# Optimization experiments

Hardware: AMD Instinct MI355X
Metric: run time of the kernel (lower is better)

The kernel has to match this reference:

```python
import jax, jax.numpy as jnp
import numpy as np
from jax import lax

B, L = 4, 1024
D_MODEL, D_STATE, D_CONV = 512, 16, 4
D_INNER = 2 * D_MODEL          # expand=2
DT_RANK = D_MODEL // 16        # ceil(512/16)=32
K_EXPERTS = 2                  # num_experts_per_token; only first k experts are used
EPS = 1e-5


def setup_inputs() -> dict:
    key = jax.random.key(0)
    ks = jax.random.split(key, 14)
    def n(k, shape, scale=0.02):
        return jax.random.normal(k, shape, jnp.float32) * scale
    # Mamba S4D-real init for A: A_log = log(1..d_state) broadcast over channels
    A_log = jnp.log(jnp.broadcast_to(jnp.arange(1, D_STATE + 1, dtype=jnp.float32), (D_INNER, D_STATE)))
    return {
        "x": jax.random.normal(ks[0], (B, L, D_MODEL), jnp.float32),
        "in_proj_w": n(ks[1], (2 * D_INNER, D_MODEL)),
        "conv_w": n(ks[2], (D_INNER, 1, D_CONV), 0.1),
        "conv_b": n(ks[3], (D_INNER,), 0.1),
        "x_proj_w": n(ks[4], (DT_RANK + 2 * D_STATE, D_INNER)),
        "dt_proj_w": n(ks[5], (D_INNER, DT_RANK), 0.1),
        "dt_proj_b": n(ks[6], (D_INNER,), 0.1),
        "A_log": A_log,
        "D_skip": jnp.ones((D_INNER,), jnp.float32),
        "out_proj_w": n(ks[7], (D_MODEL, D_INNER)),
        "moe_w1": n(ks[8], (K_EXPERTS, 2 * D_MODEL, D_MODEL)),
        "moe_b1": n(ks[9], (K_EXPERTS, 2 * D_MODEL)),
        "moe_w2": n(ks[10], (K_EXPERTS, D_MODEL, 2 * D_MODEL)),
        "moe_b2": n(ks[11], (K_EXPERTS, D_MODEL)),
    }


def _layernorm(x):
    # fresh nn.LayerNorm each forward: weight=1, bias=0, eps=1e-5
    mu = jnp.mean(x, -1, keepdims=True)
    var = jnp.mean(jnp.square(x - mu), -1, keepdims=True)
    return (x - mu) / jnp.sqrt(var + EPS)


def _mamba(x, in_proj_w, conv_w, conv_b, x_proj_w, dt_proj_w, dt_proj_b, A_log, D_skip, out_proj_w):
    b = x.shape[0]
    xz = x @ in_proj_w.T                               # (b, L, 2*d_inner)
    xc, z = jnp.split(xz, 2, axis=-1)
    # causal depthwise conv1d (torch pads both sides with d_conv-1 then slices [:L])
    conv = lax.conv_general_dilated(
        xc.transpose(0, 2, 1), conv_w, (1,), [(D_CONV - 1, 0)],
        feature_group_count=D_INNER) + conv_b[None, :, None]
    xs = jax.nn.silu(conv).transpose(0, 2, 1)          # (b, L, d_inner)
    dbc = xs @ x_proj_w.T                              # (b, L, dt_rank + 2*d_state)
    dt = dbc[..., :DT_RANK]
    Bm = dbc[..., DT_RANK:DT_RANK + D_STATE]           # (b, L, d_state)
    Cm = dbc[..., DT_RANK + D_STATE:]                  # (b, L, d_state)
    delta = jax.nn.softplus(dt @ dt_proj_w.T + dt_proj_b)  # (b, L, d_inner)
    A = -jnp.exp(A_log)                                # (d_inner, d_state)
    dA = jnp.exp(jnp.einsum('bld,dn->bldn', delta, A))     # (b, L, d_inner, d_state)
    dBx = (delta * xs)[..., None] * Bm[:, :, None, :]       # (b, L, d_inner, d_state)

    def step(h, inp):
        dA_t, dBx_t, C_t = inp
        h = dA_t * h + dBx_t                           # (b, d_inner, d_state)
        y = jnp.einsum('bdn,bn->bd', h, C_t)
        return h, y

    h0 = jnp.zeros((b, D_INNER, D_STATE), x.dtype)
    _, ys = lax.scan(step, h0, (dA.transpose(1, 0, 2, 3), dBx.transpose(1, 0, 2, 3), Cm.transpose(1, 0, 2)))
    y = ys.transpose(1, 0, 2) + xs * D_skip            # (b, L, d_inner)
    y = y * jax.nn.silu(z)
    return y @ out_proj_w.T                            # (b, L, d_model)


def reference(x, in_proj_w, conv_w, conv_b, x_proj_w, dt_proj_w, dt_proj_b,
              A_log, D_skip, out_proj_w, moe_w1, moe_b1, moe_w2, moe_b2):
    skip = x
    h = _layernorm(x)
    h = _mamba(h, in_proj_w, conv_w, conv_b, x_proj_w, dt_proj_w, dt_proj_b, A_log, D_skip, out_proj_w) + h
    h = _layernorm(h)
    # static 'MoE': unweighted average of the first K_EXPERTS dense FFNs
    a = jax.nn.relu(jnp.einsum('bld,ekd->belk', h, moe_w1) + moe_b1[None, :, None, :])
    moe = jnp.einsum('belk,edk->beld', a, moe_w2) + moe_b2[None, :, None, :]
    return jnp.mean(moe, axis=1) + skip
```

## Files before the change

kernel.cpp:

```cpp
#include <hip/hip_runtime.h>
#include <hip/hip_bf16.h>

#define BB 4
#define LL 1024
#define DM 512
#define DI 1024
#define DS 16
#define DTR 32
#define MM (BB*LL)

#define ACT_NONE 0
#define ACT_RELU 1
#define ACT_SP   2

#define CHUNK 128
#define NCH (LL/CHUNK)
#define NSTATE 65536

typedef __attribute__((ext_vector_type(8))) __bf16 bf16x8;
typedef __attribute__((ext_vector_type(8))) unsigned short us8;
typedef __attribute__((ext_vector_type(4))) float f32x4;

__device__ __forceinline__ unsigned short f2bf(float f) {
  union { float f; unsigned int u; } a; a.f = f;
  unsigned int r = a.u + 0x7fffu + ((a.u >> 16) & 1u);
  return (unsigned short)(r >> 16);
}

__device__ __forceinline__ bf16x8 ld_frag(const unsigned short* p) {
  us8 s = *(const us8*)p;
  return __builtin_bit_cast(bf16x8, s);
}

__device__ __forceinline__ void gload16(const void* g, void* l) {
  __builtin_amdgcn_global_load_lds(
      (const __attribute__((address_space(1))) void*)g,
      (__attribute__((address_space(3))) void*)l, 16, 0, 0);
}

__global__ __launch_bounds__(256) void f2b4_kernel(const float* __restrict__ in,
                                                   unsigned short* __restrict__ out, int n4) {
  int i = blockIdx.x * 256 + threadIdx.x;
  if (i < n4) {
    float4 v = ((const float4*)in)[i];
    ushort4 o;
    o.x = f2bf(v.x); o.y = f2bf(v.y); o.z = f2bf(v.z); o.w = f2bf(v.w);
    ((ushort4*)out)[i] = o;
  }
}

__global__ __launch_bounds__(256) void repack_kernel(
    const float* __restrict__ moe_w2, const float* __restrict__ moe_b2,
    unsigned short* __restrict__ w2catb, float* __restrict__ b2avg)
{
  int idx = blockIdx.x * 256 + threadIdx.x;
  if (idx < DM * 2*DI) {
    int nrow = idx >> 11;
    int t = idx & (2*DI - 1);
    int e = t >> 10;
    int k = t & (DI - 1);
    w2catb[idx] = f2bf(moe_w2[((size_t)e*DM + nrow)*DI + k]);
  }
  if (idx < DM) b2avg[idx] = 0.5f * (moe_b2[idx] + moe_b2[DM + idx]);
}

__global__ __launch_bounds__(256) void ln_kernel(const float* __restrict__ in,
                                                 float* __restrict__ outf,
                                                 unsigned short* __restrict__ outb) {
  int row = blockIdx.x;
  const float* p = in + (size_t)row * DM;
  float2 v = ((const float2*)p)[threadIdx.x];
  float s  = v.x + v.y;
  float ss = v.x*v.x + v.y*v.y;
  for (int o = 32; o; o >>= 1) { s += __shfl_down(s, o); ss += __shfl_down(ss, o); }
  __shared__ float red[8];
  int wid = threadIdx.x >> 6, lane = threadIdx.x & 63;
  if (lane == 0) { red[wid] = s; red[4+wid] = ss; }
  __syncthreads();
  s  = red[0]+red[1]+red[2]+red[3];
  ss = red[4]+red[5]+red[6]+red[7];
  float mu = s * (1.f/DM);
  float var = ss * (1.f/DM) - mu*mu;
  float rstd = rsqrtf(var + 1e-5f);
  float2 o2; o2.x = (v.x-mu)*rstd; o2.y = (v.y-mu)*rstd;
  if (outf) ((float2*)(outf + (size_t)row*DM))[threadIdx.x] = o2;
  if (outb) {
    ushort2 u; u.x = f2bf(o2.x); u.y = f2bf(o2.y);
    ((ushort2*)(outb + (size_t)row*DM))[threadIdx.x] = u;
  }
}

template<int BM, int BN, int BK, int WR, int WC, int FM, int FN, int ACT,
         bool OUTF, bool OUTB, bool DBUF>
__global__ __launch_bounds__(256) void gemm_mfma(
    const unsigned short* __restrict__ A, int lda,
    const unsigned short* __restrict__ B, int ldb,
    const float* __restrict__ bias,
    const float* __restrict__ res, int ldres,
    float* __restrict__ Cf, unsigned short* __restrict__ Cb, int ldc,
    int K, float scale, int nbx)
{
  static_assert(WR*WC == 4 && WR*FM*16 == BM && WC*FN*16 == BN, "geom");
  constexpr int ATILE = BM*BK, BTILE = BN*BK;
  constexpr int AL = ATILE/2048, BL = BTILE/2048;
  constexpr bool SWZ = (BK == 64);
  __shared__ unsigned short As[(DBUF?2:1)*ATILE];
  __shared__ unsigned short Bs[(DBUF?2:1)*BTILE];
  const int tid = threadIdx.x;
  const int nwg = gridDim.x;
  const int bid = blockIdx.x;
  const int cpx = nwg >> 3;
  const int wid = ((nwg & 7) == 0) ? ((bid & 7)*cpx + (bid >> 3)) : bid;
  const int bm = (wid / nbx) * BM;
  const int bn = (wid % nbx) * BN;
  const int w = tid >> 6, lane = tid & 63;
  const int wr = w / WC, wc = w % WC;
  const int rl = lane & 15, kg = lane >> 4;

  auto stage = [&](int buf, int k0) {
    #pragma unroll
    for (int it = 0; it < AL; ++it) {
      int o = (it*256 + tid) * 16;
      int os = SWZ ? (o ^ (((o>>7)&7)<<4)) : o;
      int e = os >> 1;
      int r = e / BK, c = e % BK;
      gload16(A + (size_t)(bm + r)*lda + k0 + c, (char*)As + buf*ATILE*2 + o);
    }
    #pragma unroll
    for (int it = 0; it < BL; ++it) {
      int o = (it*256 + tid) * 16;
      int os = SWZ ? (o ^ (((o>>7)&7)<<4)) : o;
      int e = os >> 1;
      int r = e / BK, c = e % BK;
      gload16(B + (size_t)(bn + r)*ldb + k0 + c, (char*)Bs + buf*BTILE*2 + o);
    }
  };

  f32x4 acc[FM][FN];
  #pragma unroll
  for (int m = 0; m < FM; ++m)
    #pragma unroll
    for (int n = 0; n < FN; ++n) { f32x4 z = {0.f,0.f,0.f,0.f}; acc[m][n] = z; }

  auto compute = [&](int buf) {
    #pragma unroll
    for (int kk = 0; kk < BK/32; ++kk) {
      bf16x8 af[FM], bfv[FN];
      #pragma unroll
      for (int m = 0; m < FM; ++m) {
        int byte = ((wr*FM*16 + m*16 + rl)*BK + kk*32 + kg*8) * 2;
        if (SWZ) byte ^= ((byte>>7)&7)<<4;
        af[m] = ld_frag((const unsigned short*)((const char*)As + buf*ATILE*2 + byte));
      }
      #pragma unroll
      for (int n = 0; n < FN; ++n) {
        int byte = ((wc*FN*16 + n*16 + rl)*BK + kk*32 + kg*8) * 2;
        if (SWZ) byte ^= ((byte>>7)&7)<<4;
        bfv[n] = ld_frag((const unsigned short*)((const char*)Bs + buf*BTILE*2 + byte));
      }
      #pragma unroll
      for (int m = 0; m < FM; ++m)
        #pragma unroll
        for (int n = 0; n < FN; ++n)
          acc[m][n] = __builtin_amdgcn_mfma_f32_16x16x32_bf16(af[m], bfv[n], acc[m][n], 0, 0, 0);
    }
  };

  if (DBUF) {
    stage(0, 0);
    const int nk = K / BK;
    for (int it = 0; it < nk; ++it) {
      __syncthreads();
      if (it + 1 < nk) stage((it&1)^1, (it+1)*BK);
      compute(it & 1);
    }
  } else {
    for (int k0 = 0; k0 < K; k0 += BK) {
      stage(0, k0);
      __syncthreads();
      compute(0);
      __syncthreads();
    }
  }

  #pragma unroll
  for (int m = 0; m < FM; ++m) {
    int row = bm + wr*FM*16 + m*16 + kg*4;
    #pragma unroll
    for (int n = 0; n < FN; ++n) {
      int col = bn + wc*FN*16 + n*16 + rl;
      float bv = bias ? bias[col] : 0.f;
      #pragma unroll
      for (int j = 0; j < 4; ++j) {
        float v = acc[m][n][j] * scale + bv;
        if (ACT == ACT_RELU) v = fmaxf(v, 0.f);
        if (ACT == ACT_SP)   v = fmaxf(v, 0.f) + log1pf(__expf(-fabsf(v)));
        if (res) v += res[(size_t)(row + j)*ldres + col];
        size_t off = (size_t)(row + j)*ldc + col;
        if (OUTF) Cf[off] = v;
        if (OUTB) Cb[off] = f2bf(v);
      }
    }
  }
}

__global__ __launch_bounds__(256) void conv_silu_kernel(
    const float* __restrict__ xz, const float* __restrict__ conv_w,
    const float* __restrict__ conv_b, float* __restrict__ xs,
    unsigned short* __restrict__ xsb)
{
  int gid = blockIdx.x * 256 + threadIdx.x;
  int d = gid & (DI-1);
  int l = (gid >> 10) & (LL-1);
  int b = gid >> 20;
  const float* w = conv_w + d*4;
  float s = conv_b[d];
  size_t base = (size_t)b * LL * 2*DI + d;
  #pragma unroll
  for (int k = 0; k < 4; ++k) {
    int ll = l - 3 + k;
    if (ll >= 0) s = fmaf(w[k], xz[base + (size_t)ll * 2*DI], s);
  }
  float sig = 1.f / (1.f + __expf(-s));
  float v = s * sig;
  xs[gid] = v;
  xsb[gid] = f2bf(v);
}

__global__ __launch_bounds__(256) void scan_p1(
    const float* __restrict__ delta,
    const float* __restrict__ xs,
    const float* __restrict__ dbc,
    const float* __restrict__ A_log,
    float* __restrict__ P, float* __restrict__ Q)
{
  int blk = blockIdx.x;
  int c  = blk & (NCH-1);
  int dg = (blk >> 3) & 63;
  int b  = blk >> 9;
  int tid = threadIdx.x;
  int g = tid >> 4, n = tid & 15;
  int d0 = dg*16;
  float Adn2 = -__expf(A_log[(d0+g)*DS + n]) * 1.44269504f;
  __shared__ float s_d[16][68], s_dx[16][68], s_B[16][68];
  float h = 0.f, S = 0.f;
  int lbase = c*CHUNK;
  for (int l0 = 0; l0 < CHUNK; l0 += 64) {
    {
      int li = tid >> 2, dd = (tid & 3) * 4;
      size_t row = (size_t)b*LL + lbase + l0 + li;
      float4 vd = *(const float4*)(delta + row*DI + d0 + dd);
      float4 vx = *(const float4*)(xs    + row*DI + d0 + dd);
      float4 vB = *(const float4*)(dbc   + row*64 + 32 + dd);
      s_d [dd+0][li]=vd.x; s_d [dd+1][li]=vd.y; s_d [dd+2][li]=vd.z; s_d [dd+3][li]=vd.w;
      s_dx[dd+0][li]=vd.x*vx.x; s_dx[dd+1][li]=vd.y*vx.y; s_dx[dd+2][li]=vd.z*vx.z; s_dx[dd+3][li]=vd.w*vx.w;
      s_B [dd+0][li]=vB.x; s_B [dd+1][li]=vB.y; s_B [dd+2][li]=vB.z; s_B [dd+3][li]=vB.w;
    }
    __syncthreads();
    #pragma unroll
    for (int q4 = 0; q4 < 64; q4 += 4) {
      float4 vd  = *(const float4*)&s_d[g][q4];
      float4 vdx = *(const float4*)&s_dx[g][q4];
      float4 vB  = *(const float4*)&s_B[n][q4];
      float dA;
      dA = exp2f(vd.x*Adn2); h = fmaf(dA, h, vdx.x*vB.x); S += vd.x;
      dA = exp2f(vd.y*Adn2); h = fmaf(dA, h, vdx.y*vB.y); S += vd.y;
      dA = exp2f(vd.z*Adn2); h = fmaf(dA, h, vdx.z*vB.z); S += vd.z;
      dA = exp2f(vd.w*Adn2); h = fmaf(dA, h, vdx.w*vB.w); S += vd.w;
    }
    __syncthreads();
  }
  int base = ((b*64 + dg)*256 + g*16 + n) + NSTATE*c;
  P[base] = exp2f(S * Adn2);
  Q[base] = h;
}

__global__ __launch_bounds__(256) void scan_stitch(
    const float* __restrict__ P, const float* __restrict__ Q,
    float* __restrict__ H)
{
  int t = blockIdx.x * 256 + threadIdx.x;
  float h = 0.f;
  #pragma unroll
  for (int c = 0; c < NCH; ++c) {
    H[t + NSTATE*c] = h;
    h = fmaf(P[t + NSTATE*c], h, Q[t + NSTATE*c]);
  }
}

__global__ __launch_bounds__(256) void scan_p2(
    const float* __restrict__ delta,
    const float* __restrict__ xs,
    const float* __restrict__ xz,
    const float* __restrict__ dbc,
    const float* __restrict__ A_log,
    const float* __restrict__ D_skip,
    const float* __restrict__ H,
    unsigned short* __restrict__ ymulb)
{
  int blk = blockIdx.x;
  int c  = blk & (NCH-1);
  int dg = (blk >> 3) & 63;
  int b  = blk >> 9;
  int tid = threadIdx.x;
  int g = tid >> 4, n = tid & 15;
  int d0 = dg*16;
  float Adn2 = -__expf(A_log[(d0+g)*DS + n]) * 1.44269504f;
  __shared__ float s_d[16][68], s_dx[16][68], s_B[16][68], s_C[16][68];
  __shared__ float s_z[64][17], s_t[64][17];
  __shared__ float s_yp[16][16][17];
  float h = H[((b*64 + dg)*256 + g*16 + n) + NSTATE*c];
  int lbase = c*CHUNK;
  for (int l0 = 0; l0 < CHUNK; l0 += 64) {
    {
      int li = tid >> 2, dd = (tid & 3) * 4;
      size_t row = (size_t)b*LL + lbase + l0 + li;
      float4 vd = *(const float4*)(delta + row*DI + d0 + dd);
      float4 vx = *(const float4*)(xs    + row*DI + d0 + dd);
      float4 vz = *(const float4*)(xz    + row*2*DI + DI + d0 + dd);
      float4 vB = *(const float4*)(dbc   + row*64 + 32 + dd);
      float4 vC = *(const float4*)(dbc   + row*64 + 48 + dd);
      float4 vD = *(const float4*)(D_skip + d0 + dd);
      s_d [dd+0][li]=vd.x; s_d [dd+1][li]=vd.y; s_d [dd+2][li]=vd.z; s_d [dd+3][li]=vd.w;
      s_dx[dd+0][li]=vd.x*vx.x; s_dx[dd+1][li]=vd.y*vx.y; s_dx[dd+2][li]=vd.z*vx.z; s_dx[dd+3][li]=vd.w*vx.w;
      s_B [dd+0][li]=vB.x; s_B [dd+1][li]=vB.y; s_B [dd+2][li]=vB.z; s_B [dd+3][li]=vB.w;
      s_C [dd+0][li]=vC.x; s_C [dd+1][li]=vC.y; s_C [dd+2][li]=vC.z; s_C [dd+3][li]=vC.w;
      float4 sz;
      sz.x = vz.x / (1.f + __expf(-vz.x));
      sz.y = vz.y / (1.f + __expf(-vz.y));
      sz.z = vz.z / (1.f + __expf(-vz.z));
      sz.w = vz.w / (1.f + __expf(-vz.w));
      s_z[li][dd+0]=sz.x; s_z[li][dd+1]=sz.y; s_z[li][dd+2]=sz.z; s_z[li][dd+3]=sz.w;
      s_t[li][dd+0]=vx.x*vD.x*sz.x; s_t[li][dd+1]=vx.y*vD.y*sz.y;
      s_t[li][dd+2]=vx.z*vD.z*sz.z; s_t[li][dd+3]=vx.w*vD.w*sz.w;
    }
    __syncthreads();
    #pragma unroll
    for (int sub = 0; sub < 4; ++sub) {
      #pragma unroll
      for (int q4 = 0; q4 < 16; q4 += 4) {
        int li = sub*16 + q4;
        float4 vd  = *(const float4*)&s_d[g][li];
        float4 vdx = *(const float4*)&s_dx[g][li];
        float4 vB  = *(const float4*)&s_B[n][li];
        float4 vC  = *(const float4*)&s_C[n][li];
        float dA;
        dA = exp2f(vd.x*Adn2); h = fmaf(dA, h, vdx.x*vB.x); s_yp[g][n][q4+0] = h*vC.x;
        dA = exp2f(vd.y*Adn2); h = fmaf(dA, h, vdx.y*vB.y); s_yp[g][n][q4+1] = h*vC.y;
        dA = exp2f(vd.z*Adn2); h = fmaf(dA, h, vdx.z*vB.z); s_yp[g][n][q4+2] = h*vC.z;
        dA = exp2f(vd.w*Adn2); h = fmaf(dA, h, vdx.w*vB.w); s_yp[g][n][q4+3] = h*vC.w;
      }
      __syncthreads();
      {
        int q_r = tid & 15, g_r = tid >> 4;
        float y = 0.f;
        #pragma unroll
        for (int nn = 0; nn < 16; ++nn) y += s_yp[g_r][nn][q_r];
        int lis = sub*16 + q_r;
        float v = y * s_z[lis][g_r] + s_t[lis][g_r];
        ymulb[((size_t)b*LL + lbase + l0 + lis)*DI + d0 + g_r] = f2bf(v);
      }
      __syncthreads();
    }
  }
}

extern "C" void kernel_launch(void* const* d_in, const int* in_sizes, int n_in,
                              void* d_out, int out_size, void* d_ws, size_t ws_size,
                              hipStream_t stream) {
  const float* x         = (const float*)d_in[0];
  const float* in_proj_w = (const float*)d_in[1];
  const float* conv_w    = (const float*)d_in[2];
  const float* conv_b    = (const float*)d_in[3];
  const float* x_proj_w  = (const float*)d_in[4];
  const float* dt_proj_w = (const float*)d_in[5];
  const float* dt_proj_b = (const float*)d_in[6];
  const float* A_log     = (const float*)d_in[7];
  const float* D_skip    = (const float*)d_in[8];
  const float* out_proj_w= (const float*)d_in[9];
  const float* moe_w1    = (const float*)d_in[10];
  const float* moe_b1    = (const float*)d_in[11];
  const float* moe_w2    = (const float*)d_in[12];
  const float* moe_b2    = (const float*)d_in[13];
  float* out = (float*)d_out;

  float* ws = (float*)d_ws;
  float*          h1    = ws;
  unsigned short* h1b   = (unsigned short*)(h1 + 2097152);
  float*          xz    = (float*)((float*)h1b + 1048576);
  float*          xs    = xz + 8388608;
  unsigned short* xsb   = (unsigned short*)(xs + 4194304);
  float*          delta = (float*)((float*)xsb + 2097152);
  float*          dbc   = delta + 4194304;
  unsigned short* dbcb  = (unsigned short*)(dbc + 262144);
  float*          wb    = (float*)dbcb + 131072;
  unsigned short* inpb  = (unsigned short*)wb;
  unsigned short* xpjb  = (unsigned short*)(wb + 524288);
  unsigned short* dtpb  = (unsigned short*)(wb + 524288+32768);
  unsigned short* outpb = (unsigned short*)(wb + 524288+32768+16384);
  unsigned short* w1b   = (unsigned short*)(wb + 524288+32768+16384+262144);
  unsigned short* w2cb  = (unsigned short*)(wb + 524288+32768+16384+262144+524288);
  float*          b2avg = wb + 524288+32768+16384+262144+524288+524288;
  unsigned short* ymulb = xsb;
  float*          h2    = xs;
  unsigned short* h2lnb = (unsigned short*)(xz + 4194304);
  unsigned short* acatb = (unsigned short*)xz;
  float*          Pbuf  = (float*)inpb;
  float*          Qbuf  = (float*)h1b;
  float*          Hbuf  = (float*)h1b + 524288;

  f2b4_kernel<<<(1048576/4 + 255)/256, 256, 0, stream>>>(in_proj_w, inpb, 1048576/4);
  f2b4_kernel<<<(65536/4   + 255)/256, 256, 0, stream>>>(x_proj_w,  xpjb, 65536/4);
  f2b4_kernel<<<(32768/4   + 255)/256, 256, 0, stream>>>(dt_proj_w, dtpb, 32768/4);
  f2b4_kernel<<<(524288/4  + 255)/256, 256, 0, stream>>>(out_proj_w,outpb,524288/4);
  f2b4_kernel<<<(1048576/4 + 255)/256, 256, 0, stream>>>(moe_w1,    w1b,  1048576/4);
  repack_kernel<<<(DM*2*DI + 255)/256, 256, 0, stream>>>(moe_w2, moe_b2, w2cb, b2avg);
  ln_kernel<<<MM, 256, 0, stream>>>(x, h1, h1b);
  gemm_mfma<128,128,64,2,2,4,4,ACT_NONE,true,false,true><<<512, 256, 0, stream>>>(
      h1b, DM, inpb, DM, nullptr, nullptr, 0, xz, nullptr, 2*DI, DM, 1.f, 16);
  conv_silu_kernel<<<(MM*DI)/256, 256, 0, stream>>>(xz, conv_w, conv_b, xs, xsb);
  gemm_mfma<64,64,64,2,2,2,2,ACT_NONE,true,true,true><<<64, 256, 0, stream>>>(
      xsb, DI, xpjb, DI, nullptr, nullptr, 0, dbc, dbcb, 64, DI, 1.f, 1);
  gemm_mfma<128,128,32,2,2,4,4,ACT_SP,true,false,false><<<256, 256, 0, stream>>>(
      dbcb, 64, dtpb, DTR, dt_proj_b, nullptr, 0, delta, nullptr, DI, DTR, 1.f, 8);
  scan_p1<<<BB*64*NCH, 256, 0, stream>>>(delta, xs, dbc, A_log, Pbuf, Qbuf);
  scan_stitch<<<NSTATE/256, 256, 0, stream>>>(Pbuf, Qbuf, Hbuf);
  scan_p2<<<BB*64*NCH, 256, 0, stream>>>(delta, xs, xz, dbc, A_log, D_skip, Hbuf, ymulb);
  gemm_mfma<64,64,64,2,2,2,2,ACT_NONE,true,false,true><<<512, 256, 0, stream>>>(
      ymulb, DI, outpb, DI, nullptr, h1, DM, h2, nullptr, DM, DI, 1.f, 8);
  ln_kernel<<<MM, 256, 0, stream>>>(h2, nullptr, h2lnb);
  gemm_mfma<128,128,64,2,2,4,4,ACT_RELU,false,true,true><<<512, 256, 0, stream>>>(
      h2lnb, DM, w1b, DM, moe_b1, nullptr, 0, nullptr, acatb, 2*DI, DM, 1.f, 16);
  gemm_mfma<64,64,64,2,2,2,2,ACT_NONE,true,false,true><<<512, 256, 0, stream>>>(
      acatb, 2*DI, w2cb, 2*DI, b2avg, x, DM, out, nullptr, DM, 2*DI, 0.5f, 8);
}
```

Measured before the change: 225.1 us.

## Store xz, xs and delta intermediates in bf16 and fuse weight prep kernels

The in_proj and dt_proj GEMMs now write only bf16 outputs. The conv, scan_p1 and scan_p2 kernels read these bf16 tensors instead of fp32 copies, which roughly halves the memory traffic of the memory-bound middle stages. The conv kernel is vectorised to process 8 channels per thread, and the six weight-conversion launches are merged into one prep kernel. The workspace is laid out with separate buffers instead of aliasing. This lowers precision for delta and xs inside the scan, which could add numerical error over long sequences.

```diff
diff --git a/kernel.cpp b/kernel.cpp
--- a/kernel.cpp
+++ b/kernel.cpp
@@ -26,6 +26,9 @@
   unsigned int r = a.u + 0x7fffu + ((a.u >> 16) & 1u);
   return (unsigned short)(r >> 16);
 }
+__device__ __forceinline__ float b2f(unsigned short u) {
+  union { unsigned int i; float f; } a; a.i = (unsigned int)u << 16; return a.f;
+}
 
 __device__ __forceinline__ bf16x8 ld_frag(const unsigned short* p) {
   us8 s = *(const us8*)p;
@@ -38,30 +41,44 @@
       (__attribute__((address_space(3))) void*)l, 16, 0, 0);
 }
 
-__global__ __launch_bounds__(256) void f2b4_kernel(const float* __restrict__ in,
-                                                   unsigned short* __restrict__ out, int n4) {
+__global__ __launch_bounds__(256) void prep_kernel(
+    const float* __restrict__ in_proj_w, const float* __restrict__ x_proj_w,
+    const float* __restrict__ dt_proj_w, const float* __restrict__ out_proj_w,
+    const float* __restrict__ moe_w1,    const float* __restrict__ moe_w2,
+    const float* __restrict__ moe_b2,
+    unsigned short* __restrict__ inpb,  unsigned short* __restrict__ xpjb,
+    unsigned short* __restrict__ dtpb,  unsigned short* __restrict__ outpb,
+    unsigned short* __restrict__ w1b,   unsigned short* __restrict__ w2cb,
+    float* __restrict__ b2avg)
+{
   int i = blockIdx.x * 256 + threadIdx.x;
-  if (i < n4) {
-    float4 v = ((const float4*)in)[i];
-    ushort4 o;
-    o.x = f2bf(v.x); o.y = f2bf(v.y); o.z = f2bf(v.z); o.w = f2bf(v.w);
-    ((ushort4*)out)[i] = o;
-  }
-}
-
-__global__ __launch_bounds__(256) void repack_kernel(
-    const float* __restrict__ moe_w2, const float* __restrict__ moe_b2,
-    unsigned short* __restrict__ w2catb, float* __restrict__ b2avg)
-{
-  int idx = blockIdx.x * 256 + threadIdx.x;
-  if (idx < DM * 2*DI) {
-    int nrow = idx >> 11;
-    int t = idx & (2*DI - 1);
-    int e = t >> 10;
-    int k = t & (DI - 1);
-    w2catb[idx] = f2bf(moe_w2[((size_t)e*DM + nrow)*DI + k]);
-  }
-  if (idx < DM) b2avg[idx] = 0.5f * (moe_b2[idx] + moe_b2[DM + idx]);
+  int i4 = i * 4;
+  auto cvt4 = [&](const float* src, unsigned short* dst) {
+    float4 v = ((const float4*)src)[i];
+    ushort4 o; o.x = f2bf(v.x); o.y = f2bf(v.y); o.z = f2bf(v.z); o.w = f2bf(v.w);
+    ((ushort4*)dst)[i] = o;
+  };
+  if (i4 < 2*DI*DM) cvt4(in_proj_w, inpb);
+  if (i4 < 64*DI)   cvt4(x_proj_w, xpjb);
+  if (i4 < DI*DTR)  cvt4(dt_proj_w, dtpb);
+  if (i4 < DM*DI)   cvt4(out_proj_w, outpb);
+  if (i4 < 2*DM*DM*2) cvt4(moe_w1, w1b);
+  if (i4 < DM*2*DI) {
+    #pragma unroll
+    for (int j = 0; j < 4; ++j) {
+      int idx = i4 + j;
+      int nrow = idx >> 11;
+      int t = idx & (2*DI - 1);
+      int e = t >> 10;
+      int k = t & (DI - 1);
+      w2cb[idx] = f2bf(moe_w2[((size_t)e*DM + nrow)*DI + k]);
+    }
+  }
+  if (i4 < DM) {
+    #pragma unroll
+    for (int j = 0; j < 4; ++j)
+      b2avg[i4+j] = 0.5f * (moe_b2[i4+j] + moe_b2[DM + i4+j]);
+  }
 }
 
 __global__ __launch_bounds__(256) void ln_kernel(const float* __restrict__ in,
@@ -205,31 +222,40 @@
 }
 
 __global__ __launch_bounds__(256) void conv_silu_kernel(
-    const float* __restrict__ xz, const float* __restrict__ conv_w,
-    const float* __restrict__ conv_b, float* __restrict__ xs,
-    unsigned short* __restrict__ xsb)
-{
-  int gid = blockIdx.x * 256 + threadIdx.x;
-  int d = gid & (DI-1);
-  int l = (gid >> 10) & (LL-1);
-  int b = gid >> 20;
-  const float* w = conv_w + d*4;
-  float s = conv_b[d];
-  size_t base = (size_t)b * LL * 2*DI + d;
+    const unsigned short* __restrict__ xzb, const float* __restrict__ conv_w,
+    const float* __restrict__ conv_b, unsigned short* __restrict__ xsb)
+{
+  int t = blockIdx.x * 256 + threadIdx.x;
+  int d8 = (t & (DI/8 - 1)) * 8;
+  int l = (t >> 7) & (LL-1);
+  int b = t >> 17;
+  size_t base = (size_t)(b*LL) * 2*DI + d8;
+  float acc[8];
+  #pragma unroll
+  for (int j = 0; j < 8; ++j) acc[j] = conv_b[d8+j];
   #pragma unroll
   for (int k = 0; k < 4; ++k) {
     int ll = l - 3 + k;
-    if (ll >= 0) s = fmaf(w[k], xz[base + (size_t)ll * 2*DI], s);
-  }
-  float sig = 1.f / (1.f + __expf(-s));
-  float v = s * sig;
-  xs[gid] = v;
-  xsb[gid] = f2bf(v);
+    if (ll >= 0) {
+      us8 v = *(const us8*)(xzb + base + (size_t)ll * 2*DI);
+      #pragma unroll
+      for (int j = 0; j < 8; ++j)
+        acc[j] = fmaf(conv_w[(d8+j)*4 + k], b2f((unsigned short)v[j]), acc[j]);
+    }
+  }
+  us8 o;
+  #pragma unroll
+  for (int j = 0; j < 8; ++j) {
+    float s = acc[j];
+    float v = s / (1.f + __expf(-s));
+    o[j] = (unsigned short)f2bf(v);
+  }
+  *(us8*)(xsb + (size_t)((b*LL + l)*DI) + d8) = o;
 }
 
 __global__ __launch_bounds__(256) void scan_p1(
-    const float* __restrict__ delta,
-    const float* __restrict__ xs,
+    const unsigned short* __restrict__ deltab,
+    const unsigned short* __restrict__ xsb,
     const float* __restrict__ dbc,
     const float* __restrict__ A_log,
     float* __restrict__ P, float* __restrict__ Q)
@@ -249,11 +275,13 @@
     {
       int li = tid >> 2, dd = (tid & 3) * 4;
       size_t row = (size_t)b*LL + lbase + l0 + li;
-      float4 vd = *(const float4*)(delta + row*DI + d0 + dd);
-      float4 vx = *(const float4*)(xs    + row*DI + d0 + dd);
+      ushort4 ud = *(const ushort4*)(deltab + row*DI + d0 + dd);
+      ushort4 ux = *(const ushort4*)(xsb    + row*DI + d0 + dd);
       float4 vB = *(const float4*)(dbc   + row*64 + 32 + dd);
-      s_d [dd+0][li]=vd.x; s_d [dd+1][li]=vd.y; s_d [dd+2][li]=vd.z; s_d [dd+3][li]=vd.w;
-      s_dx[dd+0][li]=vd.x*vx.x; s_dx[dd+1][li]=vd.y*vx.y; s_dx[dd+2][li]=vd.z*vx.z; s_dx[dd+3][li]=vd.w*vx.w;
+      float dx_ = b2f(ud.x), dy_ = b2f(ud.y), dz_ = b2f(ud.z), dw_ = b2f(ud.w);
+      float xx_ = b2f(ux.x), xy_ = b2f(ux.y), xz_ = b2f(ux.z), xw_ = b2f(ux.w);
+      s_d [dd+0][li]=dx_; s_d [dd+1][li]=dy_; s_d [dd+2][li]=dz_; s_d [dd+3][li]=dw_;
+      s_dx[dd+0][li]=dx_*xx_; s_dx[dd+1][li]=dy_*xy_; s_dx[dd+2][li]=dz_*xz_; s_dx[dd+3][li]=dw_*xw_;
       s_B [dd+0][li]=vB.x; s_B [dd+1][li]=vB.y; s_B [dd+2][li]=vB.z; s_B [dd+3][li]=vB.w;
     }
     __syncthreads();
@@ -289,9 +317,9 @@
 }
 
 __global__ __launch_bounds__(256) void scan_p2(
-    const float* __restrict__ delta,
-    const float* __restrict__ xs,
-    const float* __restrict__ xz,
+    const unsigned short* __restrict__ deltab,
+    const unsigned short* __restrict__ xsb,
+    const unsigned short* __restrict__ xzb,
     const float* __restrict__ dbc,
     const float* __restrict__ A_log,
     const float* __restrict__ D_skip,
@@ -315,24 +343,26 @@
     {
       int li = tid >> 2, dd = (tid & 3) * 4;
       size_t row = (size_t)b*LL + lbase + l0 + li;
-      float4 vd = *(const float4*)(delta + row*DI + d0 + dd);
-      float4 vx = *(const float4*)(xs    + row*DI + d0 + dd);
-      float4 vz = *(const float4*)(xz    + row*2*DI + DI + d0 + dd);
+      ushort4 ud = *(const ushort4*)(deltab + row*DI + d0 + dd);
+      ushort4 ux = *(const ushort4*)(xsb    + row*DI + d0 + dd);
+      ushort4 uz = *(const ushort4*)(xzb    + row*2*DI + DI + d0 + dd);
       float4 vB = *(const float4*)(dbc   + row*64 + 32 + dd);
       float4 vC = *(const float4*)(dbc   + row*64 + 48 + dd);
       float4 vD = *(const float4*)(D_skip + d0 + dd);
-      s_d [dd+0][li]=vd.x; s_d [dd+1][li]=vd.y; s_d [dd+2][li]=vd.z; s_d [dd+3][li]=vd.w;
-      s_dx[dd+0][li]=vd.x*vx.x; s_dx[dd+1][li]=vd.y*vx.y; s_dx[dd+2][li]=vd.z*vx.z; s_dx[dd+3][li]=vd.w*vx.w;
+      float dx_ = b2f(ud.x), dy_ = b2f(ud.y), dz_ = b2f(ud.z), dw_ = b2f(ud.w);
+      float xx_ = b2f(ux.x), xy_ = b2f(ux.y), xz2 = b2f(ux.z), xw_ = b2f(ux.w);
+      float zx_ = b2f(uz.x), zy_ = b2f(uz.y), zz_ = b2f(uz.z), zw_ = b2f(uz.w);
+      s_d [dd+0][li]=dx_; s_d [dd+1][li]=dy_; s_d [dd+2][li]=dz_; s_d [dd+3][li]=dw_;
+      s_dx[dd+0][li]=dx_*xx_; s_dx[dd+1][li]=dy_*xy_; s_dx[dd+2][li]=dz_*xz2; s_dx[dd+3][li]=dw_*xw_;
       s_B [dd+0][li]=vB.x; s_B [dd+1][li]=vB.y; s_B [dd+2][li]=vB.z; s_B [dd+3][li]=vB.w;
       s_C [dd+0][li]=vC.x; s_C [dd+1][li]=vC.y; s_C [dd+2][li]=vC.z; s_C [dd+3][li]=vC.w;
-      float4 sz;
-      sz.x = vz.x / (1.f + __expf(-vz.x));
-      sz.y = vz.y / (1.f + __expf(-vz.y));
-      sz.z = vz.z / (1.f + __expf(-vz.z));
-      sz.w = vz.w / (1.f + __expf(-vz.w));
-      s_z[li][dd+0]=sz.x; s_z[li][dd+1]=sz.y; s_z[li][dd+2]=sz.z; s_z[li][dd+3]=sz.w;
-      s_t[li][dd+0]=vx.x*vD.x*sz.x; s_t[li][dd+1]=vx.y*vD.y*sz.y;
-      s_t[li][dd+2]=vx.z*vD.z*sz.z; s_t[li][dd+3]=vx.w*vD.w*sz.w;
+      float szx = zx_ / (1.f + __expf(-zx_));
+      float szy = zy_ / (1.f + __expf(-zy_));
+      float szz = zz_ / (1.f + __expf(-zz_));
+      float szw = zw_ / (1.f + __expf(-zw_));
+      s_z[li][dd+0]=szx; s_z[li][dd+1]=szy; s_z[li][dd+2]=szz; s_z[li][dd+3]=szw;
+      s_t[li][dd+0]=xx_*vD.x*szx; s_t[li][dd+1]=xy_*vD.y*szy;
+      s_t[li][dd+2]=xz2*vD.z*szz; s_t[li][dd+3]=xw_*vD.w*szw;
     }
     __syncthreads();
     #pragma unroll
@@ -384,48 +414,43 @@
   const float* moe_b2    = (const float*)d_in[13];
   float* out = (float*)d_out;
 
-  float* ws = (float*)d_ws;
-  float*          h1    = ws;
-  unsigned short* h1b   = (unsigned short*)(h1 + 2097152);
-  float*          xz    = (float*)((float*)h1b + 1048576);
-  float*          xs    = xz + 8388608;
-  unsigned short* xsb   = (unsigned short*)(xs + 4194304);
-  float*          delta = (float*)((float*)xsb + 2097152);
-  float*          dbc   = delta + 4194304;
-  unsigned short* dbcb  = (unsigned short*)(dbc + 262144);
-  float*          wb    = (float*)dbcb + 131072;
-  unsigned short* inpb  = (unsigned short*)wb;
-  unsigned short* xpjb  = (unsigned short*)(wb + 524288);
-  unsigned short* dtpb  = (unsigned short*)(wb + 524288+32768);
-  unsigned short* outpb = (unsigned short*)(wb + 524288+32768+16384);
-  unsigned short* w1b   = (unsigned short*)(wb + 524288+32768+16384+262144);
-  unsigned short* w2cb  = (unsigned short*)(wb + 524288+32768+16384+262144+524288);
-  float*          b2avg = wb + 524288+32768+16384+262144+524288+524288;
-  unsigned short* ymulb = xsb;
-  float*          h2    = xs;
-  unsigned short* h2lnb = (unsigned short*)(xz + 4194304);
-  unsigned short* acatb = (unsigned short*)xz;
-  float*          Pbuf  = (float*)inpb;
-  float*          Qbuf  = (float*)h1b;
-  float*          Hbuf  = (float*)h1b + 524288;
-
-  f2b4_kernel<<<(1048576/4 + 255)/256, 256, 0, stream>>>(in_proj_w, inpb, 1048576/4);
-  f2b4_kernel<<<(65536/4   + 255)/256, 256, 0, stream>>>(x_proj_w,  xpjb, 65536/4);
-  f2b4_kernel<<<(32768/4   + 255)/256, 256, 0, stream>>>(dt_proj_w, dtpb, 32768/4);
-  f2b4_kernel<<<(524288/4  + 255)/256, 256, 0, stream>>>(out_proj_w,outpb,524288/4);
-  f2b4_kernel<<<(1048576/4 + 255)/256, 256, 0, stream>>>(moe_w1,    w1b,  1048576/4);
-  repack_kernel<<<(DM*2*DI + 255)/256, 256, 0, stream>>>(moe_w2, moe_b2, w2cb, b2avg);
+  float* p = (float*)d_ws;
+  float* h1    = p; p += 2097152;
+  float* h2    = p; p += 2097152;
+  float* dbc   = p; p += 262144;
+  float* Pbuf  = p; p += NSTATE*NCH/1;
+  float* Qbuf  = p; p += 524288;
+  float* Hbuf  = p; p += 524288;
+  float* b2avg = p; p += 1024;
+  unsigned short* h1b    = (unsigned short*)p; p += 1048576;
+  unsigned short* xzb    = (unsigned short*)p; p += 4194304;
+  unsigned short* xsb    = (unsigned short*)p; p += 2097152;
+  unsigned short* deltab = (unsigned short*)p; p += 2097152;
+  unsigned short* dbcb   = (unsigned short*)p; p += 131072;
+  unsigned short* ymulb  = (unsigned short*)p; p += 2097152;
+  unsigned short* h2lnb  = (unsigned short*)p; p += 1048576;
+  unsigned short* acatb  = (unsigned short*)p; p += 4194304;
+  unsigned short* inpb   = (unsigned short*)p; p += 524288;
+  unsigned short* xpjb   = (unsigned short*)p; p += 32768;
+  unsigned short* dtpb   = (unsigned short*)p; p += 16384;
+  unsigned short* outpb  = (unsigned short*)p; p += 262144;
+  unsigned short* w1b    = (unsigned short*)p; p += 524288;
+  unsigned short* w2cb   = (unsigned short*)p; p += 524288;
+
+  prep_kernel<<<1024, 256, 0, stream>>>(in_proj_w, x_proj_w, dt_proj_w, out_proj_w,
+                                        moe_w1, moe_w2, moe_b2,
+                                        inpb, xpjb, dtpb, outpb, w1b, w2cb, b2avg);
   ln_kernel<<<MM, 256, 0, stream>>>(x, h1, h1b);
-  gemm_mfma<128,128,64,2,2,4,4,ACT_NONE,true,false,true><<<512, 256, 0, stream>>>(
-      h1b, DM, inpb, DM, nullptr, nullptr, 0, xz, nullptr, 2*DI, DM, 1.f, 16);
-  conv_silu_kernel<<<(MM*DI)/256, 256, 0, stream>>>(xz, conv_w, conv_b, xs, xsb);
+  gemm_mfma<128,128,64,2,2,4,4,ACT_NONE,false,true,true><<<512, 256, 0, stream>>>(
+      h1b, DM, inpb, DM, nullptr, nullptr, 0, nullptr, xzb, 2*DI, DM, 1.f, 16);
+  conv_silu_kernel<<<(MM*DI/8)/256, 256, 0, stream>>>(xzb, conv_w, conv_b, xsb);
   gemm_mfma<64,64,64,2,2,2,2,ACT_NONE,true,true,true><<<64, 256, 0, stream>>>(
       xsb, DI, xpjb, DI, nullptr, nullptr, 0, dbc, dbcb, 64, DI, 1.f, 1);
-  gemm_mfma<128,128,32,2,2,4,4,ACT_SP,true,false,false><<<256, 256, 0, stream>>>(
-      dbcb, 64, dtpb, DTR, dt_proj_b, nullptr, 0, delta, nullptr, DI, DTR, 1.f, 8);
-  scan_p1<<<BB*64*NCH, 256, 0, stream>>>(delta, xs, dbc, A_log, Pbuf, Qbuf);
+  gemm_mfma<128,128,32,2,2,4,4,ACT_SP,false,true,false><<<256, 256, 0, stream>>>(
+      dbcb, 64, dtpb, DTR, dt_proj_b, nullptr, 0, nullptr, deltab, DI, DTR, 1.f, 8);
+  scan_p1<<<BB*64*NCH, 256, 0, stream>>>(deltab, xsb, dbc, A_log, Pbuf, Qbuf);
   scan_stitch<<<NSTATE/256, 256, 0, stream>>>(Pbuf, Qbuf, Hbuf);
-  scan_p2<<<BB*64*NCH, 256, 0, stream>>>(delta, xs, xz, dbc, A_log, D_skip, Hbuf, ymulb);
+  scan_p2<<<BB*64*NCH, 256, 0, stream>>>(deltab, xsb, xzb, dbc, A_log, D_skip, Hbuf, ymulb);
   gemm_mfma<64,64,64,2,2,2,2,ACT_NONE,true,false,true><<<512, 256, 0, stream>>>(
       ymulb, DI, outpb, DI, nullptr, h1, DM, h2, nullptr, DM, DI, 1.f, 8);
   ln_kernel<<<MM, 256, 0, stream>>>(h2, nullptr, h2lnb);
```

After: 221.4 us. No clear change (-1.7%).
